# Kernel tuning notes

Hardware: AMD Instinct MI355X
Metric: run time of the kernel (lower is better)

The kernel has to match this reference:

```python
import jax, jax.numpy as jnp
import numpy as np

EMB = 1024
DM = 64
NH = 16

def setup_inputs() -> dict:
    key = jax.random.key(0)
    ks = jax.random.split(key, 11)
    bs, slen = 2, 2048
    s = 1.0 / np.sqrt(EMB)
    inp = {
        'Q': jax.random.normal(ks[0], (bs, slen, EMB), jnp.float32),
        'K': jax.random.normal(ks[1], (bs, slen, EMB), jnp.float32),
        'V': jax.random.normal(ks[2], (bs, slen, EMB), jnp.float32),
        'Wq': jax.random.normal(ks[3], (EMB, DM * NH), jnp.float32) * s,
        'bq': jnp.zeros((DM * NH,), jnp.float32),
        'Wk': jax.random.normal(ks[4], (EMB, DM * NH), jnp.float32) * s,
        'bk': jnp.zeros((DM * NH,), jnp.float32),
        'Wv': jax.random.normal(ks[5], (EMB, DM * NH), jnp.float32) * s,
        'bv': jnp.zeros((DM * NH,), jnp.float32),
        'Wo': jax.random.normal(ks[6], (DM * NH, EMB), jnp.float32) * (1.0 / np.sqrt(DM * NH)),
        'bo': jnp.zeros((EMB,), jnp.float32),
    }
    return inp

def reference(Q, K, V, Wq, bq, Wk, bk, Wv, bv, Wo, bo):
    bs, q_len, _ = Q.shape
    kv_len = K.shape[1]
    scale = 1.0 / np.sqrt(DM)
    # project and split heads: (n, l, h, d)
    q = (scale * (Q @ Wq + bq)).reshape(bs, q_len, NH, DM)
    k = (K @ Wk + bk).reshape(bs, kv_len, NH, DM)
    v = (V @ Wv + bv).reshape(bs, kv_len, NH, DM)
    # scores (n, h, l, s) -- full S x S matrix, as in the original
    qk = jnp.einsum('nlhd,nshd->nhls', q, k)
    a = jax.nn.softmax(qk, axis=-1)  # dropout p=0 -> identity
    o = jnp.einsum('nhls,nshd->nlhd', a, v).reshape(bs, q_len, NH * DM)
    return o @ Wo + bo
```

## Files before the change

### kernel.cpp

```cpp
#include <hip/hip_runtime.h>
#include <cstdint>
#include <cstddef>

#define EMB  1024
#define DM   64
#define NH   16
#define SLEN 2048
#define BS   2

typedef _Float16 f16x8 __attribute__((ext_vector_type(8)));
typedef _Float16 f16x4 __attribute__((ext_vector_type(4)));
typedef float    f32x4 __attribute__((ext_vector_type(4)));

#define ASYNC_LD16(gp, lp)                                                        \
    __builtin_amdgcn_global_load_lds(                                             \
        (const __attribute__((address_space(1))) void*)(gp),                      \
        (__attribute__((address_space(3))) void*)(lp), 16, 0, 0)

__global__ __launch_bounds__(256)
void prep(const float* __restrict__ Q, const float* __restrict__ K,
          const float* __restrict__ V,
          const float* __restrict__ Wq, const float* __restrict__ Wk,
          const float* __restrict__ Wv, const float* __restrict__ Wo,
          _Float16* __restrict__ Qh, _Float16* __restrict__ Kh,
          _Float16* __restrict__ Vh,
          _Float16* __restrict__ WqT, _Float16* __restrict__ WkT,
          _Float16* __restrict__ WvT, _Float16* __restrict__ WoT)
{
    __shared__ float t[64][65];
    const int z = blockIdx.z;
    if (z < 3) {
        const float* in  = (z == 0) ? Q : (z == 1) ? K : V;
        _Float16*    out = (z == 0) ? Qh : (z == 1) ? Kh : Vh;
        size_t i = ((size_t)blockIdx.x * 256 + threadIdx.x) * 8;
        float4 a = *(const float4*)(in + i);
        float4 b = *(const float4*)(in + i + 4);
        f16x8 o;
        o[0] = (_Float16)a.x; o[1] = (_Float16)a.y; o[2] = (_Float16)a.z; o[3] = (_Float16)a.w;
        o[4] = (_Float16)b.x; o[5] = (_Float16)b.y; o[6] = (_Float16)b.z; o[7] = (_Float16)b.w;
        *(f16x8*)(out + i) = o;
        return;
    }
    if (blockIdx.x >= 256) return;
    const float* W;
    _Float16*    T;
    switch (z - 3) {
        case 0:  W = Wq; T = WqT; break;
        case 1:  W = Wk; T = WkT; break;
        case 2:  W = Wv; T = WvT; break;
        default: W = Wo; T = WoT; break;
    }
    const int tid = threadIdx.x;
    const int bn  = (blockIdx.x & 15) * 64;
    const int bk  = (blockIdx.x >> 4) * 64;

    #pragma unroll
    for (int p = 0; p < 4; ++p) {
        int row = p * 16 + (tid >> 4);
        int col = (tid & 15) * 4;
        float4 v = *(const float4*)(W + (size_t)(bk + row) * EMB + bn + col);
        t[row][col+0] = v.x; t[row][col+1] = v.y; t[row][col+2] = v.z; t[row][col+3] = v.w;
    }
    __syncthreads();
    #pragma unroll
    for (int p = 0; p < 4; ++p) {
        int nr = p * 16 + (tid >> 4);
        int kc = (tid & 15) * 4;
        f16x4 o;
        o[0] = (_Float16)t[kc+0][nr];
        o[1] = (_Float16)t[kc+1][nr];
        o[2] = (_Float16)t[kc+2][nr];
        o[3] = (_Float16)t[kc+3][nr];
        *(f16x4*)&T[(size_t)(bn + nr) * EMB + bk + kc] = o;
    }
}

__device__ __forceinline__
void gemm_core(const _Float16* __restrict__ A, const _Float16* __restrict__ Bt,
               const float* __restrict__ bias, float* __restrict__ Cf,
               _Float16* __restrict__ Ch, int M, int N, int K,
               float scale, int mode, int bx, int by)
{
    __shared__ __align__(16) _Float16 As[128 * 32];
    __shared__ __align__(16) _Float16 Bs[128 * 32];

    const int tid  = threadIdx.x;
    const int lane = tid & 63;
    const int wave = tid >> 6;
    const int c    = lane & 15;
    const int quad = lane >> 4;
    const int bm   = by * 128;
    const int bn   = bx * 128;
    const int wm   = (wave >> 1) * 64;
    const int wn   = (wave & 1) * 64;

    f32x4 acc[4][4];
    #pragma unroll
    for (int i = 0; i < 4; ++i)
        #pragma unroll
        for (int j = 0; j < 4; ++j)
            #pragma unroll
            for (int r = 0; r < 4; ++r) acc[i][j][r] = 0.f;

    const char* gA = (const char*)(A + (size_t)(bm + (tid >> 2)) * K) + (tid & 3) * 16;
    const char* gB = (const char*)(Bt + (size_t)(bn + (tid >> 2)) * K) + (tid & 3) * 16;
    char* lA = (char*)As + wave * 1024;
    char* lB = (char*)Bs + wave * 1024;
    const size_t rowskip = (size_t)64 * K * 2;

    for (int k0 = 0; k0 < K; k0 += 32) {
        __syncthreads();
        ASYNC_LD16(gA + (size_t)k0 * 2,           lA);
        ASYNC_LD16(gA + rowskip + (size_t)k0 * 2, lA + 4096);
        ASYNC_LD16(gB + (size_t)k0 * 2,           lB);
        ASYNC_LD16(gB + rowskip + (size_t)k0 * 2, lB + 4096);
        __syncthreads();

        f16x8 af[4], bf[4];
        #pragma unroll
        for (int i = 0; i < 4; ++i)
            af[i] = *(const f16x8*)&As[(wm + i * 16 + c) * 32 + quad * 8];
        #pragma unroll
        for (int j = 0; j < 4; ++j)
            bf[j] = *(const f16x8*)&Bs[(wn + j * 16 + c) * 32 + quad * 8];

        #pragma unroll
        for (int i = 0; i < 4; ++i)
            #pragma unroll
            for (int j = 0; j < 4; ++j)
                acc[i][j] = __builtin_amdgcn_mfma_f32_16x16x32_f16(af[i], bf[j], acc[i][j], 0, 0, 0);
    }

    float bcol[4];
    #pragma unroll
    for (int j = 0; j < 4; ++j) bcol[j] = bias[bn + wn + j * 16 + c];

    #pragma unroll
    for (int i = 0; i < 4; ++i) {
        int m0 = bm + wm + i * 16 + quad * 4;
        #pragma unroll
        for (int j = 0; j < 4; ++j) {
            int n = bn + wn + j * 16 + c;
            if (mode == 0) {
                #pragma unroll
                for (int r = 0; r < 4; ++r)
                    Cf[(size_t)(m0 + r) * N + n] = acc[i][j][r] + bcol[j];
            } else if (mode == 1) {
                int h = n >> 6, d = n & 63;
                #pragma unroll
                for (int r = 0; r < 4; ++r) {
                    int mm = m0 + r;
                    int b = mm >> 11, l = mm & (SLEN - 1);
                    Ch[(((size_t)(b * NH + h)) * SLEN + l) * DM + d] =
                        (_Float16)((acc[i][j][r] + bcol[j]) * scale);
                }
            } else {
                int h = n >> 6, d = n & 63;
                int b = m0 >> 11, l = m0 & (SLEN - 1);
                f16x4 o;
                #pragma unroll
                for (int r = 0; r < 4; ++r)
                    o[r] = (_Float16)(acc[i][j][r] + bcol[j]);
                *(f16x4*)&Ch[(((size_t)(b * NH + h)) * DM + d) * SLEN + l] = o;
            }
        }
    }
}

__global__ __launch_bounds__(256)
void gemm_qkv(const _Float16* __restrict__ Qh, const _Float16* __restrict__ Kh,
              const _Float16* __restrict__ Vh,
              const _Float16* __restrict__ WqT, const _Float16* __restrict__ WkT,
              const _Float16* __restrict__ WvT,
              const float* __restrict__ bq, const float* __restrict__ bk,
              const float* __restrict__ bv,
              _Float16* __restrict__ q_ws, _Float16* __restrict__ k_ws,
              _Float16* __restrict__ v_ws)
{
    const _Float16 *A, *Bt;
    const float* bias;
    _Float16* Ch;
    float scale;
    int mode;
    if (blockIdx.z == 0)      { A = Qh; Bt = WqT; bias = bq; Ch = q_ws; scale = 0.18033688f; mode = 1; }
    else if (blockIdx.z == 1) { A = Kh; Bt = WkT; bias = bk; Ch = k_ws; scale = 1.0f;        mode = 1; }
    else                      { A = Vh; Bt = WvT; bias = bv; Ch = v_ws; scale = 1.0f;        mode = 2; }
    gemm_core(A, Bt, bias, nullptr, Ch, BS * SLEN, NH * DM, EMB, scale, mode,
              blockIdx.x, blockIdx.y);
}

__global__ __launch_bounds__(256)
void gemm_out(const _Float16* __restrict__ Oh, const _Float16* __restrict__ WoT,
              const float* __restrict__ bo, float* __restrict__ out)
{
    gemm_core(Oh, WoT, bo, out, nullptr, BS * SLEN, EMB, NH * DM, 1.0f, 0,
              blockIdx.x, blockIdx.y);
}

__global__ __launch_bounds__(256, 2)
void attn_mfma(const _Float16* __restrict__ qw, const _Float16* __restrict__ kw,
               const _Float16* __restrict__ vwT,
               float* __restrict__ Opart, float* __restrict__ lpart)
{
    __shared__ __align__(16) _Float16 Kt[2][64 * 64];
    __shared__ __align__(16) _Float16 Vt[2][64 * 64];

    const int tid  = threadIdx.x;
    const int lane = tid & 63;
    const int wave = tid >> 6;
    const int c    = lane & 15;
    const int quad = lane >> 4;
    const int bh   = blockIdx.y;
    const int kz   = blockIdx.z;
    const int qbase = blockIdx.x * 128 + wave * 32;

    const _Float16* kb = kw  + (size_t)bh * SLEN * DM + (size_t)kz * 1024 * DM;
    const _Float16* vb = vwT + (size_t)bh * DM * SLEN + (size_t)kz * 1024;
    const _Float16* qb = qw  + (size_t)bh * SLEN * DM;

    f16x8 qf[2][2];
    #pragma unroll
    for (int t = 0; t < 2; ++t)
        #pragma unroll
        for (int ch = 0; ch < 2; ++ch)
            qf[t][ch] = *(const f16x8*)(qb + (size_t)(qbase + t*16 + c) * DM + ch*32 + quad*8);

    f32x4 oacc[2][4];
    f32x4 lacc[2];
    #pragma unroll
    for (int t = 0; t < 2; ++t) {
        #pragma unroll
        for (int dg = 0; dg < 4; ++dg)
            #pragma unroll
            for (int r = 0; r < 4; ++r) oacc[t][dg][r] = 0.f;
        #pragma unroll
        for (int r = 0; r < 4; ++r) lacc[t][r] = 0.f;
    }

    const f16x4 onesf = {(_Float16)1.f, (_Float16)1.f, (_Float16)1.f, (_Float16)1.f};

    const int srow  = tid >> 3;
    const int scol  = (tid & 7) * 8;
    const int sphys = (((tid & 7) ^ (srow & 7)) * 8);

    {
        f16x8 k0 = *(const f16x8*)(kb + (size_t)srow * DM + scol);
        f16x8 k1 = *(const f16x8*)(kb + (size_t)(32 + srow) * DM + scol);
        f16x8 v0 = *(const f16x8*)(vb + (size_t)srow * SLEN + scol);
        f16x8 v1 = *(const f16x8*)(vb + (size_t)(32 + srow) * SLEN + scol);
        *(f16x8*)&Kt[0][srow * 64 + sphys]        = k0;
        *(f16x8*)&Kt[0][(32 + srow) * 64 + sphys] = k1;
        *(f16x8*)&Vt[0][srow * 64 + sphys]        = v0;
        *(f16x8*)&Vt[0][(32 + srow) * 64 + sphys] = v1;
    }
    __syncthreads();

    const int NT = 1024 / 64;
    for (int it = 0; it < NT; ++it) {
        const int cur = it & 1;
        const bool more = (it + 1 < NT);

        f16x8 kr0, kr1, vr0, vr1;
        if (more) {
            int s1 = (it + 1) * 64;
            kr0 = *(const f16x8*)(kb + (size_t)(s1 + srow) * DM + scol);
            kr1 = *(const f16x8*)(kb + (size_t)(s1 + 32 + srow) * DM + scol);
            vr0 = *(const f16x8*)(vb + (size_t)srow * SLEN + s1 + scol);
            vr1 = *(const f16x8*)(vb + (size_t)(32 + srow) * SLEN + s1 + scol);
        }

        f16x8 kf[4][2];
        #pragma unroll
        for (int g = 0; g < 4; ++g)
            #pragma unroll
            for (int ch = 0; ch < 2; ++ch)
                kf[g][ch] = *(const f16x8*)
                    &Kt[cur][(g*16 + c) * 64 + (((ch*4 + quad) ^ (c & 7)) * 8)];

        const f32x4 zero4 = {0.f, 0.f, 0.f, 0.f};
        f32x4 s[2][4];
        #pragma unroll
        for (int t = 0; t < 2; ++t)
            #pragma unroll
            for (int g = 0; g < 4; ++g) {
                s[t][g] = __builtin_amdgcn_mfma_f32_16x16x32_f16(kf[g][0], qf[t][0], zero4,   0, 0, 0);
                s[t][g] = __builtin_amdgcn_mfma_f32_16x16x32_f16(kf[g][1], qf[t][1], s[t][g], 0, 0, 0);
            }

        f16x4 pf[2][4];
        #pragma unroll
        for (int t = 0; t < 2; ++t)
            #pragma unroll
            for (int g = 0; g < 4; ++g) {
                f16x4 pv;
                pv[0] = (_Float16)exp2f(s[t][g][0]);
                pv[1] = (_Float16)exp2f(s[t][g][1]);
                pv[2] = (_Float16)exp2f(s[t][g][2]);
                pv[3] = (_Float16)exp2f(s[t][g][3]);
                pf[t][g] = pv;
            }

        #pragma unroll
        for (int g = 0; g < 4; ++g) {
            lacc[0] = __builtin_amdgcn_mfma_f32_16x16x16f16(pf[0][g], onesf, lacc[0], 0, 0, 0);
            lacc[1] = __builtin_amdgcn_mfma_f32_16x16x16f16(pf[1][g], onesf, lacc[1], 0, 0, 0);
        }

        #pragma unroll
        for (int dg = 0; dg < 4; ++dg) {
            f16x4 vf[4];
            #pragma unroll
            for (int g = 0; g < 4; ++g)
                vf[g] = *(const f16x4*)
                    &Vt[cur][(dg*16 + c) * 64 +
                             (((2*g + (quad >> 1)) ^ (c & 7)) * 8) + (quad & 1) * 4];
            #pragma unroll
            for (int g = 0; g < 4; ++g)
                #pragma unroll
                for (int t = 0; t < 2; ++t)
                    oacc[t][dg] = __builtin_amdgcn_mfma_f32_16x16x16f16(pf[t][g], vf[g], oacc[t][dg], 0, 0, 0);
        }

        if (more) {
            int nb = cur ^ 1;
            *(f16x8*)&Kt[nb][srow * 64 + sphys]        = kr0;
            *(f16x8*)&Kt[nb][(32 + srow) * 64 + sphys] = kr1;
            *(f16x8*)&Vt[nb][srow * 64 + sphys]        = vr0;
            *(f16x8*)&Vt[nb][(32 + srow) * 64 + sphys] = vr1;
        }
        __syncthreads();
    }

    const size_t pbase = ((size_t)kz * 32 + bh) * SLEN;
    #pragma unroll
    for (int t = 0; t < 2; ++t) {
        if (c == 0) {
            #pragma unroll
            for (int r = 0; r < 4; ++r)
                lpart[pbase + qbase + t*16 + quad*4 + r] = lacc[t][r];
        }
        #pragma unroll
        for (int r = 0; r < 4; ++r) {
            int row = qbase + t*16 + quad*4 + r;
            #pragma unroll
            for (int dg = 0; dg < 4; ++dg)
                Opart[(pbase + row) * 64 + dg*16 + c] = oacc[t][dg][r];
        }
    }
}

__global__ __launch_bounds__(256)
void attn_merge(const float* __restrict__ Opart, const float* __restrict__ lpart,
                _Float16* __restrict__ ow)
{
    size_t idx = ((size_t)blockIdx.x * 256 + threadIdx.x) * 4;
    int bh  = (int)(idx >> 17);
    int rem = (int)(idx & 131071);
    int row = rem >> 6, d = rem & 63;
    float4 o0 = *(const float4*)(Opart + idx);
    float4 o1 = *(const float4*)(Opart + (1u << 22) + idx);
    float l = lpart[(size_t)bh * SLEN + row] + lpart[65536 + (size_t)bh * SLEN + row];
    float inv = 1.0f / l;
    int b = bh >> 4, h = bh & 15;
    f16x4 o;
    o[0] = (_Float16)((o0.x + o1.x) * inv);
    o[1] = (_Float16)((o0.y + o1.y) * inv);
    o[2] = (_Float16)((o0.z + o1.z) * inv);
    o[3] = (_Float16)((o0.w + o1.w) * inv);
    *(f16x4*)&ow[((size_t)b * SLEN + row) * EMB + h * DM + d] = o;
}

extern "C" void kernel_launch(void* const* d_in, const int* in_sizes, int n_in,
                              void* d_out, int out_size, void* d_ws, size_t ws_size,
                              hipStream_t stream)
{
    const float* Q  = (const float*)d_in[0];
    const float* K  = (const float*)d_in[1];
    const float* V  = (const float*)d_in[2];
    const float* Wq = (const float*)d_in[3];
    const float* bq = (const float*)d_in[4];
    const float* Wk = (const float*)d_in[5];
    const float* bk = (const float*)d_in[6];
    const float* Wv = (const float*)d_in[7];
    const float* bv = (const float*)d_in[8];
    const float* Wo = (const float*)d_in[9];
    const float* bo = (const float*)d_in[10];
    float* out = (float*)d_out;

    const size_t MN = (size_t)BS * SLEN * NH * DM;
    const size_t WW = (size_t)EMB * NH * DM;

    _Float16* base = (_Float16*)d_ws;
    _Float16* Qh   = base;
    _Float16* Kh   = Qh  + MN;
    _Float16* Vh   = Kh  + MN;
    _Float16* WqT  = Vh  + MN;
    _Float16* WkT  = WqT + WW;
    _Float16* WvT  = WkT + WW;
    _Float16* WoT  = base + 16 * 1024 * 1024;
    _Float16* q_ws = WoT + WW;
    _Float16* k_ws = q_ws + MN;
    _Float16* v_ws = k_ws + MN;
    _Float16* o_ws = v_ws + MN;
    float*    lpart = (float*)(o_ws + MN);
    float*    Opart = (float*)d_ws;

    dim3 blk(256);

    prep<<<dim3(2048, 1, 7), blk, 0, stream>>>(Q, K, V, Wq, Wk, Wv, Wo,
                                               Qh, Kh, Vh, WqT, WkT, WvT, WoT);

    gemm_qkv<<<dim3(8, 32, 3), blk, 0, stream>>>(Qh, Kh, Vh, WqT, WkT, WvT,
                                                 bq, bk, bv, q_ws, k_ws, v_ws);

    attn_mfma<<<dim3(SLEN / 128, BS * NH, 2), blk, 0, stream>>>(q_ws, k_ws, v_ws,
                                                                Opart, lpart);

    attn_merge<<<dim3(4096), blk, 0, stream>>>(Opart, lpart, o_ws);

    gemm_out<<<dim3(8, 32, 1), blk, 0, stream>>>(o_ws, WoT, bo, out);
}
```

Baseline: 244.0 us.

## Fuse split-KV merge into attention kernel and use async global-to-LDS loads

```diff
diff --git a/kernel.cpp b/kernel.cpp
--- a/kernel.cpp
+++ b/kernel.cpp
@@ -10,6 +10,8 @@
 
 typedef _Float16 f16x8 __attribute__((ext_vector_type(8)));
 typedef _Float16 f16x4 __attribute__((ext_vector_type(4)));
+typedef __fp16   hf2   __attribute__((ext_vector_type(2)));
+typedef __fp16   hf4   __attribute__((ext_vector_type(4)));
 typedef float    f32x4 __attribute__((ext_vector_type(4)));
 
 #define ASYNC_LD16(gp, lp)                                                        \
@@ -197,10 +199,9 @@
               blockIdx.x, blockIdx.y);
 }
 
-__global__ __launch_bounds__(256, 2)
+__global__ __launch_bounds__(256)
 void attn_mfma(const _Float16* __restrict__ qw, const _Float16* __restrict__ kw,
-               const _Float16* __restrict__ vwT,
-               float* __restrict__ Opart, float* __restrict__ lpart)
+               const _Float16* __restrict__ vwT, _Float16* __restrict__ ow)
 {
     __shared__ __align__(16) _Float16 Kt[2][64 * 64];
     __shared__ __align__(16) _Float16 Vt[2][64 * 64];
@@ -211,11 +212,12 @@
     const int c    = lane & 15;
     const int quad = lane >> 4;
     const int bh   = blockIdx.y;
-    const int kz   = blockIdx.z;
+    const int b    = bh >> 4;
+    const int h    = bh & 15;
     const int qbase = blockIdx.x * 128 + wave * 32;
 
-    const _Float16* kb = kw  + (size_t)bh * SLEN * DM + (size_t)kz * 1024 * DM;
-    const _Float16* vb = vwT + (size_t)bh * DM * SLEN + (size_t)kz * 1024;
+    const _Float16* kb = kw  + (size_t)bh * SLEN * DM;
+    const _Float16* vb = vwT + (size_t)bh * DM * SLEN;
     const _Float16* qb = qw  + (size_t)bh * SLEN * DM;
 
     f16x8 qf[2][2];
@@ -236,37 +238,32 @@
         #pragma unroll
         for (int r = 0; r < 4; ++r) lacc[t][r] = 0.f;
     }
-
     const f16x4 onesf = {(_Float16)1.f, (_Float16)1.f, (_Float16)1.f, (_Float16)1.f};
-
-    const int srow  = tid >> 3;
-    const int scol  = (tid & 7) * 8;
-    const int sphys = (((tid & 7) ^ (srow & 7)) * 8);
-
-    {
-        f16x8 k0 = *(const f16x8*)(kb + (size_t)srow * DM + scol);
-        f16x8 k1 = *(const f16x8*)(kb + (size_t)(32 + srow) * DM + scol);
-        f16x8 v0 = *(const f16x8*)(vb + (size_t)srow * SLEN + scol);
-        f16x8 v1 = *(const f16x8*)(vb + (size_t)(32 + srow) * SLEN + scol);
-        *(f16x8*)&Kt[0][srow * 64 + sphys]        = k0;
-        *(f16x8*)&Kt[0][(32 + srow) * 64 + sphys] = k1;
-        *(f16x8*)&Vt[0][srow * 64 + sphys]        = v0;
-        *(f16x8*)&Vt[0][(32 + srow) * 64 + sphys] = v1;
-    }
+    const f32x4 zero4 = {0.f, 0.f, 0.f, 0.f};
+
+    const int r0  = wave * 16 + (lane >> 3);
+    const int lc0 = (((lane & 7) ^ (r0 & 7)) * 16);
+    const char* gk = (const char*)kb + r0 * 128 + lc0;
+    const char* gv = (const char*)vb + (size_t)r0 * 4096 + lc0;
+    char* lK = (char*)&Kt[0][0] + wave * 2048;
+    char* lV = (char*)&Vt[0][0] + wave * 2048;
+
+    ASYNC_LD16(gk,         lK);
+    ASYNC_LD16(gk + 1024,  lK + 1024);
+    ASYNC_LD16(gv,         lV);
+    ASYNC_LD16(gv + 32768, lV + 1024);
+    gk += 8192; gv += 128;
     __syncthreads();
 
-    const int NT = 1024 / 64;
-    for (int it = 0; it < NT; ++it) {
-        const int cur = it & 1;
-        const bool more = (it + 1 < NT);
-
-        f16x8 kr0, kr1, vr0, vr1;
-        if (more) {
-            int s1 = (it + 1) * 64;
-            kr0 = *(const f16x8*)(kb + (size_t)(s1 + srow) * DM + scol);
-            kr1 = *(const f16x8*)(kb + (size_t)(s1 + 32 + srow) * DM + scol);
-            vr0 = *(const f16x8*)(vb + (size_t)srow * SLEN + s1 + scol);
-            vr1 = *(const f16x8*)(vb + (size_t)(32 + srow) * SLEN + s1 + scol);
+    auto tile = [&](int cur) {
+        {
+            char* pk = (char*)&Kt[cur ^ 1][0] + wave * 2048;
+            char* pv = (char*)&Vt[cur ^ 1][0] + wave * 2048;
+            ASYNC_LD16(gk,         pk);
+            ASYNC_LD16(gk + 1024,  pk + 1024);
+            ASYNC_LD16(gv,         pv);
+            ASYNC_LD16(gv + 32768, pv + 1024);
+            gk += 8192; gv += 128;
         }
 
         f16x8 kf[4][2];
@@ -277,7 +274,6 @@
                 kf[g][ch] = *(const f16x8*)
                     &Kt[cur][(g*16 + c) * 64 + (((ch*4 + quad) ^ (c & 7)) * 8)];
 
-        const f32x4 zero4 = {0.f, 0.f, 0.f, 0.f};
         f32x4 s[2][4];
         #pragma unroll
         for (int t = 0; t < 2; ++t)
@@ -292,12 +288,14 @@
         for (int t = 0; t < 2; ++t)
             #pragma unroll
             for (int g = 0; g < 4; ++g) {
-                f16x4 pv;
-                pv[0] = (_Float16)exp2f(s[t][g][0]);
-                pv[1] = (_Float16)exp2f(s[t][g][1]);
-                pv[2] = (_Float16)exp2f(s[t][g][2]);
-                pv[3] = (_Float16)exp2f(s[t][g][3]);
-                pf[t][g] = pv;
+                float p0 = __builtin_amdgcn_exp2f(s[t][g][0]);
+                float p1 = __builtin_amdgcn_exp2f(s[t][g][1]);
+                float p2 = __builtin_amdgcn_exp2f(s[t][g][2]);
+                float p3 = __builtin_amdgcn_exp2f(s[t][g][3]);
+                hf2 lo = __builtin_amdgcn_cvt_pkrtz(p0, p1);
+                hf2 hi = __builtin_amdgcn_cvt_pkrtz(p2, p3);
+                hf4 pv = __builtin_shufflevector(lo, hi, 0, 1, 2, 3);
+                pf[t][g] = __builtin_bit_cast(f16x4, pv);
             }
 
         #pragma unroll
@@ -320,54 +318,26 @@
                 for (int t = 0; t < 2; ++t)
                     oacc[t][dg] = __builtin_amdgcn_mfma_f32_16x16x16f16(pf[t][g], vf[g], oacc[t][dg], 0, 0, 0);
         }
-
-        if (more) {
-            int nb = cur ^ 1;
-            *(f16x8*)&Kt[nb][srow * 64 + sphys]        = kr0;
-            *(f16x8*)&Kt[nb][(32 + srow) * 64 + sphys] = kr1;
-            *(f16x8*)&Vt[nb][srow * 64 + sphys]        = vr0;
-            *(f16x8*)&Vt[nb][(32 + srow) * 64 + sphys] = vr1;
-        }
         __syncthreads();
-    }
-
-    const size_t pbase = ((size_t)kz * 32 + bh) * SLEN;
+    };
+
+    for (int it = 0; it < SLEN / 64; it += 2) {
+        tile(0);
+        tile(1);
+    }
+
     #pragma unroll
     for (int t = 0; t < 2; ++t) {
-        if (c == 0) {
-            #pragma unroll
-            for (int r = 0; r < 4; ++r)
-                lpart[pbase + qbase + t*16 + quad*4 + r] = lacc[t][r];
-        }
         #pragma unroll
         for (int r = 0; r < 4; ++r) {
+            float linv = 1.0f / lacc[t][r];
             int row = qbase + t*16 + quad*4 + r;
             #pragma unroll
             for (int dg = 0; dg < 4; ++dg)
-                Opart[(pbase + row) * 64 + dg*16 + c] = oacc[t][dg][r];
-        }
-    }
-}
-
-__global__ __launch_bounds__(256)
-void attn_merge(const float* __restrict__ Opart, const float* __restrict__ lpart,
-                _Float16* __restrict__ ow)
-{
-    size_t idx = ((size_t)blockIdx.x * 256 + threadIdx.x) * 4;
-    int bh  = (int)(idx >> 17);
-    int rem = (int)(idx & 131071);
-    int row = rem >> 6, d = rem & 63;
-    float4 o0 = *(const float4*)(Opart + idx);
-    float4 o1 = *(const float4*)(Opart + (1u << 22) + idx);
-    float l = lpart[(size_t)bh * SLEN + row] + lpart[65536 + (size_t)bh * SLEN + row];
-    float inv = 1.0f / l;
-    int b = bh >> 4, h = bh & 15;
-    f16x4 o;
-    o[0] = (_Float16)((o0.x + o1.x) * inv);
-    o[1] = (_Float16)((o0.y + o1.y) * inv);
-    o[2] = (_Float16)((o0.z + o1.z) * inv);
-    o[3] = (_Float16)((o0.w + o1.w) * inv);
-    *(f16x4*)&ow[((size_t)b * SLEN + row) * EMB + h * DM + d] = o;
+                ow[((size_t)b * SLEN + row) * EMB + h * DM + dg*16 + c] =
+                    (_Float16)(oacc[t][dg][r] * linv);
+        }
+    }
 }
 
 extern "C" void kernel_launch(void* const* d_in, const int* in_sizes, int n_in,
@@ -397,13 +367,11 @@
     _Float16* WqT  = Vh  + MN;
     _Float16* WkT  = WqT + WW;
     _Float16* WvT  = WkT + WW;
-    _Float16* WoT  = base + 16 * 1024 * 1024;
+    _Float16* WoT  = WvT + WW;
     _Float16* q_ws = WoT + WW;
     _Float16* k_ws = q_ws + MN;
     _Float16* v_ws = k_ws + MN;
     _Float16* o_ws = v_ws + MN;
-    float*    lpart = (float*)(o_ws + MN);
-    float*    Opart = (float*)d_ws;
 
     dim3 blk(256);
 
@@ -413,10 +381,7 @@
     gemm_qkv<<<dim3(8, 32, 3), blk, 0, stream>>>(Qh, Kh, Vh, WqT, WkT, WvT,
                                                  bq, bk, bv, q_ws, k_ws, v_ws);
 
-    attn_mfma<<<dim3(SLEN / 128, BS * NH, 2), blk, 0, stream>>>(q_ws, k_ws, v_ws,
-                                                                Opart, lpart);
-
-    attn_merge<<<dim3(4096), blk, 0, stream>>>(Opart, lpart, o_ws);
+    attn_mfma<<<dim3(SLEN / 128, BS * NH), blk, 0, stream>>>(q_ws, k_ws, v_ws, o_ws);
 
     gemm_out<<<dim3(8, 32, 1), blk, 0, stream>>>(o_ws, WoT, bo, out);
 }
```

Result: faster. 236.9 us (-2.9%).
